# Kernel optimization log

Measured on AMD Instinct MI355X. Metric: run time of the kernel, lower is better.

Reference implementation:

```python
import jax, jax.numpy as jnp
import numpy as np
import math

B, T, C = 8, 2048, 1024
N_LAYER, LAYER_ID = 24, 12


def setup_inputs() -> dict:
    key = jax.random.key(0)
    ks = jax.random.split(key, 8)
    # deterministic parameter init, mirroring RWKV_TimeMix.__init__
    ratio_0_to_1 = LAYER_ID / (N_LAYER - 1)
    ratio_1_to_almost0 = 1.0 - LAYER_ID / N_LAYER
    h = np.arange(C, dtype=np.float64)
    time_decay = (-5 + 8 * (h / (C - 1)) ** (0.7 + 1.3 * ratio_0_to_1)).astype(np.float32)
    zigzag = (np.array([(i + 1) % 3 - 1 for i in range(C)], dtype=np.float64) * 0.5)
    time_first = (np.ones(C) * math.log(0.3) + zigzag).astype(np.float32)
    xpos = (np.arange(C, dtype=np.float64) / C)
    time_mix_k = (xpos ** ratio_1_to_almost0).astype(np.float32).reshape(1, 1, C)
    time_mix_v = (xpos ** ratio_1_to_almost0 + 0.3 * ratio_0_to_1).astype(np.float32).reshape(1, 1, C)
    time_mix_r = (xpos ** (0.5 * ratio_1_to_almost0)).astype(np.float32).reshape(1, 1, C)
    scale = 1.0 / math.sqrt(C)
    return {
        "x": jax.random.normal(ks[0], (B, T, C), jnp.float32),
        "time_decay": jnp.asarray(time_decay),
        "time_first": jnp.asarray(time_first),
        "time_mix_k": jnp.asarray(time_mix_k),
        "time_mix_v": jnp.asarray(time_mix_v),
        "time_mix_r": jnp.asarray(time_mix_r),
        "Wk": jax.random.normal(ks[1], (C, C), jnp.float32) * scale,
        "Wv": jax.random.normal(ks[2], (C, C), jnp.float32) * scale,
        "Wr": jax.random.normal(ks[3], (C, C), jnp.float32) * scale,
        "Wo": jax.random.normal(ks[4], (C, C), jnp.float32) * scale,
    }


def wkv_scan(w_decay, u, k, v):
    """Numerically-stable RWKV-4 WKV recurrence.
    w_decay, u: [C]; k, v: [B, T, C]. Returns [B, T, C].
    """
    w = -jnp.exp(w_decay)  # negative decay per channel
    kt = jnp.swapaxes(k, 0, 1)  # [T, B, C]
    vt = jnp.swapaxes(v, 0, 1)
    Bn, Cn = k.shape[0], k.shape[2]
    aa0 = jnp.zeros((Bn, Cn), k.dtype)
    bb0 = jnp.zeros((Bn, Cn), k.dtype)
    pp0 = jnp.full((Bn, Cn), -1e38, k.dtype)

    def step(carry, kv):
        aa, bb, pp = carry
        k_t, v_t = kv
        ww = u + k_t
        q = jnp.maximum(pp, ww)
        e1 = jnp.exp(pp - q)
        e2 = jnp.exp(ww - q)
        y = (e1 * aa + e2 * v_t) / (e1 * bb + e2)
        ww2 = pp + w
        q2 = jnp.maximum(ww2, k_t)
        e1 = jnp.exp(ww2 - q2)
        e2 = jnp.exp(k_t - q2)
        return (e1 * aa + e2 * v_t, e1 * bb + e2, q2), y

    _, ys = jax.lax.scan(step, (aa0, bb0, pp0), (kt, vt))
    return jnp.swapaxes(ys, 0, 1)  # [B, T, C]


def reference(x, time_decay, time_first, time_mix_k, time_mix_v, time_mix_r, Wk, Wv, Wr, Wo):
    # time shift: x_{t-1}, zero at t=0
    xx = jnp.pad(x, ((0, 0), (1, 0), (0, 0)))[:, :-1]
    xk = x * time_mix_k + xx * (1.0 - time_mix_k)
    xv = x * time_mix_v + xx * (1.0 - time_mix_v)
    xr = x * time_mix_r + xx * (1.0 - time_mix_r)
    k = jnp.einsum("btc,oc->bto", xk, Wk)
    v = jnp.einsum("btc,oc->bto", xv, Wv)
    r = jnp.einsum("btc,oc->bto", xr, Wr)
    wkv = wkv_scan(time_decay, time_first, k, v)
    rwkv = jax.nn.sigmoid(r) * wkv
    return jnp.einsum("btc,oc->bto", rwkv, Wo)
```

## Files before the change

kernel.cpp:

```cpp
#include <hip/hip_runtime.h>

#define BB 8
#define TT 2048
#define CC 1024
#define WKV_L 64
#define WKV_NCH (TT / WKV_L)

typedef __bf16 bf16x8_t __attribute__((ext_vector_type(8)));
typedef float f32x4_t __attribute__((ext_vector_type(4)));

__device__ __forceinline__ unsigned short f2bf(float f) {
  unsigned u = __float_as_uint(f);
  u += 0x7fffu + ((u >> 16) & 1u);
  return (unsigned short)(u >> 16);
}
__device__ __forceinline__ float bf2f(unsigned short s) {
  return __uint_as_float(((unsigned)s) << 16);
}

#define GLOAD16(gp, lp)                                                        \
  __builtin_amdgcn_global_load_lds(                                            \
      (const __attribute__((address_space(1))) void*)(gp),                     \
      (__attribute__((address_space(3))) void*)(lp), 16, 0, 0)

__global__ __launch_bounds__(256) void mix2_cast_kernel(
    const float* __restrict__ x, const float* __restrict__ tmk,
    const float* __restrict__ tmv,
    unsigned short* __restrict__ xk, unsigned short* __restrict__ xv) {
  const size_t total4 = (size_t)BB * TT * CC / 4;
  for (size_t i = (size_t)blockIdx.x * blockDim.x + threadIdx.x; i < total4;
       i += (size_t)gridDim.x * blockDim.x) {
    size_t e = i * 4;
    int c = (int)(e & (CC - 1));
    int t = (int)((e / CC) & (TT - 1));
    float4 xv4 = ((const float4*)x)[i];
    float4 xp = make_float4(0.f, 0.f, 0.f, 0.f);
    if (t > 0) xp = ((const float4*)x)[i - CC / 4];
    float4 mk = *(const float4*)(tmk + c);
    float4 mv = *(const float4*)(tmv + c);
    ushort4 ok, ov;
    ok.x = f2bf(xv4.x * mk.x + xp.x * (1.f - mk.x));
    ok.y = f2bf(xv4.y * mk.y + xp.y * (1.f - mk.y));
    ok.z = f2bf(xv4.z * mk.z + xp.z * (1.f - mk.z));
    ok.w = f2bf(xv4.w * mk.w + xp.w * (1.f - mk.w));
    ov.x = f2bf(xv4.x * mv.x + xp.x * (1.f - mv.x));
    ov.y = f2bf(xv4.y * mv.y + xp.y * (1.f - mv.y));
    ov.z = f2bf(xv4.z * mv.z + xp.z * (1.f - mv.z));
    ov.w = f2bf(xv4.w * mv.w + xp.w * (1.f - mv.w));
    *(ushort4*)(xk + e) = ok;
    *(ushort4*)(xv + e) = ov;
  }
}

__global__ __launch_bounds__(256) void mix_cast_kernel(const float* __restrict__ x,
                                const float* __restrict__ tmix,
                                unsigned short* __restrict__ out) {
  const size_t total4 = (size_t)BB * TT * CC / 4;
  for (size_t i = (size_t)blockIdx.x * blockDim.x + threadIdx.x; i < total4;
       i += (size_t)gridDim.x * blockDim.x) {
    size_t e = i * 4;
    int c = (int)(e & (CC - 1));
    int t = (int)((e / CC) & (TT - 1));
    float4 xv = ((const float4*)x)[i];
    float4 xp = make_float4(0.f, 0.f, 0.f, 0.f);
    if (t > 0) xp = ((const float4*)x)[i - CC / 4];
    float4 tm = *(const float4*)(tmix + c);
    ushort4 o;
    o.x = f2bf(xv.x * tm.x + xp.x * (1.f - tm.x));
    o.y = f2bf(xv.y * tm.y + xp.y * (1.f - tm.y));
    o.z = f2bf(xv.z * tm.z + xp.z * (1.f - tm.z));
    o.w = f2bf(xv.w * tm.w + xp.w * (1.f - tm.w));
    *(ushort4*)(out + e) = o;
  }
}

__global__ __launch_bounds__(256) void cast_w4_kernel(
    const float* __restrict__ w0, const float* __restrict__ w1,
    const float* __restrict__ w2, const float* __restrict__ w3,
    unsigned short* __restrict__ o0, unsigned short* __restrict__ o1,
    unsigned short* __restrict__ o2, unsigned short* __restrict__ o3) {
  const int n4 = CC * CC / 4;
  for (int i = blockIdx.x * blockDim.x + threadIdx.x; i < 4 * n4;
       i += gridDim.x * blockDim.x) {
    int sel = i / n4;
    int j = i - sel * n4;
    const float* w = sel == 0 ? w0 : sel == 1 ? w1 : sel == 2 ? w2 : w3;
    unsigned short* o = sel == 0 ? o0 : sel == 1 ? o1 : sel == 2 ? o2 : o3;
    float4 v = ((const float4*)w)[j];
    ushort4 u;
    u.x = f2bf(v.x); u.y = f2bf(v.y); u.z = f2bf(v.z); u.w = f2bf(v.w);
    ((ushort4*)o)[j] = u;
  }
}

#define NT8 (CC / 64)

template <typename EPI>
__device__ __forceinline__ void gemm8_body(unsigned short* lds8,
                                           const unsigned short* __restrict__ A,
                                           const unsigned short* __restrict__ Bm,
                                           int tm, int tn, EPI epi) {
  const int tid = threadIdx.x;
  const int lane = tid & 63;
  const int wid = tid >> 6;
  const int wr = wid >> 2;
  const int wc = wid & 3;
  const int fr = lane & 15;
  const int fk = lane >> 4;

  const int srow = tid >> 3;
  const int gcol = (((tid & 7) ^ (srow & 7)) << 3);
  const unsigned short* Ag = A + (size_t)(tm * 256 + srow) * CC + gcol;
  const unsigned short* Bg = Bm + (size_t)(tn * 256 + srow) * CC + gcol;
  const int ldst = tid << 3;

  const int rowA = wr * 16 + fr;
  const int rowB = wc * 16 + fr;
  const int sx0 = ((fk ^ (fr & 7)) << 3);
  const int sx1 = (((4 + fk) ^ (fr & 7)) << 3);

  bf16x8_t aF[4][2];
  bf16x8_t bF[2][2][2];
  f32x4_t acc[8][4] = {};

#define STG_A(T, H)                                                            \
  {                                                                            \
    const unsigned short* g_ = Ag + (size_t)((H) * 128) * CC + (T) * 64;       \
    unsigned short* l_ = &lds8[(((T) & 1) << 14) + (H) * 8192 + ldst];         \
    GLOAD16(g_, l_);                                                           \
    GLOAD16(g_ + (size_t)64 * CC, l_ + 4096);                                  \
  }
#define STG_B(T, H)                                                            \
  {                                                                            \
    const unsigned short* g_ = Bg + (size_t)((H) * 128) * CC + (T) * 64;       \
    unsigned short* l_ = &lds8[32768 + (((T) & 1) << 14) + (H) * 8192 + ldst]; \
    GLOAD16(g_, l_);                                                           \
    GLOAD16(g_ + (size_t)64 * CC, l_ + 4096);                                  \
  }
#define LOADA(MH)                                                              \
  _Pragma("unroll") for (int i_ = 0; i_ < 4; ++i_) {                           \
    aF[i_][0] = *(const bf16x8_t*)&lds8[ab + ((MH) * 4 + i_) * 2048 + sx0];    \
    aF[i_][1] = *(const bf16x8_t*)&lds8[ab + ((MH) * 4 + i_) * 2048 + sx1];    \
  }
#define LOADB(NH)                                                              \
  _Pragma("unroll") for (int j_ = 0; j_ < 2; ++j_) {                           \
    bF[NH][j_][0] = *(const bf16x8_t*)&lds8[bb + ((NH) * 2 + j_) * 4096 + sx0];\
    bF[NH][j_][1] = *(const bf16x8_t*)&lds8[bb + ((NH) * 2 + j_) * 4096 + sx1];\
  }
#define MFMAQ(MH, NH)                                                          \
  _Pragma("unroll") for (int i_ = 0; i_ < 4; ++i_)                             \
  _Pragma("unroll") for (int j_ = 0; j_ < 2; ++j_) {                           \
    acc[(MH) * 4 + i_][(NH) * 2 + j_] = __builtin_amdgcn_mfma_f32_16x16x32_bf16( \
        aF[i_][0], bF[NH][j_][0], acc[(MH) * 4 + i_][(NH) * 2 + j_], 0, 0, 0); \
    acc[(MH) * 4 + i_][(NH) * 2 + j_] = __builtin_amdgcn_mfma_f32_16x16x32_bf16( \
        aF[i_][1], bF[NH][j_][1], acc[(MH) * 4 + i_][(NH) * 2 + j_], 0, 0, 0); \
  }

  STG_A(0, 0) STG_B(0, 0) STG_A(0, 1) STG_B(0, 1)
  STG_A(1, 0) STG_B(1, 0) STG_A(1, 1)
  asm volatile("s_waitcnt vmcnt(10)" ::: "memory");
  __builtin_amdgcn_s_barrier();

#pragma unroll
  for (int t = 0; t < NT8; ++t) {
    const int ab = ((t & 1) << 14) + rowA * 64;
    const int bb = 32768 + ((t & 1) << 14) + rowB * 64;
    LOADA(0) LOADB(0)
    if (t + 1 < NT8) { STG_B(t + 1, 1) }
    asm volatile("s_waitcnt vmcnt(8)" ::: "memory");
    __builtin_amdgcn_s_barrier();
    __builtin_amdgcn_s_setprio(1);
    MFMAQ(0, 0)
    __builtin_amdgcn_s_setprio(0);
    __builtin_amdgcn_s_barrier();
    LOADB(1)
    if (t + 2 < NT8) { STG_A(t + 2, 0) }
    __builtin_amdgcn_s_barrier();
    __builtin_amdgcn_s_setprio(1);
    MFMAQ(0, 1)
    __builtin_amdgcn_s_setprio(0);
    __builtin_amdgcn_s_barrier();
    LOADA(1)
    if (t + 2 < NT8) { STG_B(t + 2, 0) }
    __builtin_amdgcn_s_barrier();
    __builtin_amdgcn_s_setprio(1);
    MFMAQ(1, 0)
    __builtin_amdgcn_s_setprio(0);
    __builtin_amdgcn_s_barrier();
    if (t + 2 < NT8) { STG_A(t + 2, 1) }
    asm volatile("s_waitcnt vmcnt(10)" ::: "memory");
    __builtin_amdgcn_s_barrier();
    __builtin_amdgcn_s_setprio(1);
    MFMAQ(1, 1)
    __builtin_amdgcn_s_setprio(0);
    __builtin_amdgcn_s_barrier();
  }

#pragma unroll
  for (int im = 0; im < 8; ++im)
#pragma unroll
    for (int jn = 0; jn < 4; ++jn)
#pragma unroll
      for (int rg = 0; rg < 4; ++rg)
        epi((size_t)(tm * 256 + wr * 16 + im * 32 + (fk << 2) + rg) * CC +
                (size_t)(tn * 256 + wc * 16 + jn * 64 + fr),
            acc[im][jn][rg]);
#undef STG_A
#undef STG_B
#undef LOADA
#undef LOADB
#undef MFMAQ
}

template <int OUT_BF16>
__global__ __launch_bounds__(512, 2) void gemm8_one(const unsigned short* __restrict__ A,
                         const unsigned short* __restrict__ Bm,
                         void* __restrict__ Cm) {
  __shared__ unsigned short lds8[65536];
  int orig = blockIdx.x;
  int wg = (orig & 7) * 32 + (orig >> 3);
  int tm = wg >> 2;
  int tn = wg & 3;
  if (OUT_BF16)
    gemm8_body(lds8, A, Bm, tm, tn,
               [&](size_t off, float val) { ((unsigned short*)Cm)[off] = f2bf(val); });
  else
    gemm8_body(lds8, A, Bm, tm, tn,
               [&](size_t off, float val) { ((float*)Cm)[off] = val; });
}

__global__ __launch_bounds__(256) void wkv_phase1(const float* __restrict__ k,
                           const unsigned short* __restrict__ v,
                           const float* __restrict__ wdec,
                           float* __restrict__ Sa, float* __restrict__ Sb,
                           float* __restrict__ Sp) {
  int idx = blockIdx.x * blockDim.x + threadIdx.x;
  int c = idx & (CC - 1);
  int bj = idx >> 10;
  int j = bj % WKV_NCH;
  int b = bj / WKV_NCH;
  float w = -__expf(wdec[c]);
  size_t base = (size_t)b * TT * CC + (size_t)j * WKV_L * CC + c;
  float aa = 0.f, bb = 0.f, pp = -1e38f;
  for (int t = 0; t < WKV_L; ++t) {
    size_t off = base + (size_t)t * CC;
    float kt = k[off];
    float vt = bf2f(v[off]);
    float ww2 = pp + w;
    float q2 = fmaxf(ww2, kt);
    float f1 = __expf(ww2 - q2);
    float f2 = __expf(kt - q2);
    aa = fmaf(f1, aa, f2 * vt);
    bb = fmaf(f1, bb, f2);
    pp = q2;
  }
  Sa[idx] = aa; Sb[idx] = bb; Sp[idx] = pp;
}

__global__ __launch_bounds__(256) void wkv_phase2(const float* __restrict__ wdec,
                           const float* __restrict__ Sa, const float* __restrict__ Sb,
                           const float* __restrict__ Sp,
                           float* __restrict__ Ia, float* __restrict__ Ib,
                           float* __restrict__ Ip) {
  int idx = blockIdx.x * blockDim.x + threadIdx.x;
  if (idx >= BB * CC) return;
  int c = idx & (CC - 1);
  int b = idx >> 10;
  float wL = -__expf(wdec[c]) * (float)WKV_L;
  float aa = 0.f, bb = 0.f, pp = -1e38f;
  for (int j = 0; j < WKV_NCH; ++j) {
    size_t s = (size_t)(b * WKV_NCH + j) * CC + c;
    Ia[s] = aa; Ib[s] = bb; Ip[s] = pp;
    float pd = pp + wL;
    float ps = Sp[s];
    float q = fmaxf(pd, ps);
    float e1 = __expf(pd - q);
    float e2 = __expf(ps - q);
    aa = fmaf(e1, aa, e2 * Sa[s]);
    bb = fmaf(e1, bb, e2 * Sb[s]);
    pp = q;
  }
}

__global__ __launch_bounds__(256) void wkv_phase3(const float* __restrict__ k,
                           const unsigned short* __restrict__ v,
                           const unsigned short* r,
                           const float* __restrict__ wdec,
                           const float* __restrict__ u,
                           const float* __restrict__ Ia, const float* __restrict__ Ib,
                           const float* __restrict__ Ip,
                           unsigned short* out) {
  int idx = blockIdx.x * blockDim.x + threadIdx.x;
  int c = idx & (CC - 1);
  int bj = idx >> 10;
  int j = bj % WKV_NCH;
  int b = bj / WKV_NCH;
  float w = -__expf(wdec[c]);
  float uu = u[c];
  float aa = Ia[idx], bb = Ib[idx], pp = Ip[idx];
  size_t base = (size_t)b * TT * CC + (size_t)j * WKV_L * CC + c;
  for (int t = 0; t < WKV_L; ++t) {
    size_t off = base + (size_t)t * CC;
    float kt = k[off];
    float vt = bf2f(v[off]);
    float ww = uu + kt;
    float q = fmaxf(pp, ww);
    float e1 = __expf(pp - q);
    float e2 = __expf(ww - q);
    float y = fmaf(e1, aa, e2 * vt) / fmaf(e1, bb, e2);
    float ww2 = pp + w;
    float q2 = fmaxf(ww2, kt);
    float f1 = __expf(ww2 - q2);
    float f2 = __expf(kt - q2);
    aa = fmaf(f1, aa, f2 * vt);
    bb = fmaf(f1, bb, f2);
    pp = q2;
    float rt = bf2f(r[off]);
    float sr = 1.f / (1.f + __expf(-rt));
    out[off] = f2bf(sr * y);
  }
}

extern "C" void kernel_launch(void* const* d_in, const int* in_sizes, int n_in,
                              void* d_out, int out_size, void* d_ws, size_t ws_size,
                              hipStream_t stream) {
  const float* x    = (const float*)d_in[0];
  const float* tdec = (const float*)d_in[1];
  const float* tfir = (const float*)d_in[2];
  const float* tmk  = (const float*)d_in[3];
  const float* tmv  = (const float*)d_in[4];
  const float* tmr  = (const float*)d_in[5];
  const float* Wk   = (const float*)d_in[6];
  const float* Wv   = (const float*)d_in[7];
  const float* Wr   = (const float*)d_in[8];
  const float* Wo   = (const float*)d_in[9];

  const size_t M = (size_t)BB * TT;
  const size_t mixbytes = M * CC * 2;
  const size_t wbytes = (size_t)CC * CC * 2;
  const size_t nstate = (size_t)BB * WKV_NCH * CC;

  char* ws = (char*)d_ws;
  unsigned short* xkb = (unsigned short*)ws;  ws += mixbytes;
  unsigned short* xvb = (unsigned short*)ws;  ws += mixbytes;
  unsigned short* rbuf = xvb;
  unsigned short* Wkb = (unsigned short*)ws; ws += wbytes;
  unsigned short* Wvb = (unsigned short*)ws; ws += wbytes;
  unsigned short* Wrb = (unsigned short*)ws; ws += wbytes;
  unsigned short* Wob = (unsigned short*)ws; ws += wbytes;
  float* kbuf = (float*)ws;                   ws += M * CC * 4;
  unsigned short* vbuf = (unsigned short*)ws; ws += mixbytes;
  float* Sa = (float*)ws; ws += nstate * 4;
  float* Sb = (float*)ws; ws += nstate * 4;
  float* Sp = (float*)ws; ws += nstate * 4;
  float* Ia = (float*)ws; ws += nstate * 4;
  float* Ib = (float*)ws; ws += nstate * 4;
  float* Ip = (float*)ws; ws += nstate * 4;

  dim3 blk(256);
  dim3 blk8(512);
  const int wkv_grid = (int)(nstate / 256);

  cast_w4_kernel<<<1024, blk, 0, stream>>>(Wk, Wv, Wr, Wo, Wkb, Wvb, Wrb, Wob);
  mix2_cast_kernel<<<2048, blk, 0, stream>>>(x, tmk, tmv, xkb, xvb);
  gemm8_one<0><<<256, blk8, 0, stream>>>(xkb, Wkb, kbuf);
  gemm8_one<1><<<256, blk8, 0, stream>>>(xvb, Wvb, vbuf);
  mix_cast_kernel<<<2048, blk, 0, stream>>>(x, tmr, xkb);
  gemm8_one<1><<<256, blk8, 0, stream>>>(xkb, Wrb, rbuf);

  wkv_phase1<<<wkv_grid, blk, 0, stream>>>(kbuf, vbuf, tdec, Sa, Sb, Sp);
  wkv_phase2<<<(BB * CC + 255) / 256, blk, 0, stream>>>(tdec, Sa, Sb, Sp, Ia, Ib, Ip);
  wkv_phase3<<<wkv_grid, blk, 0, stream>>>(kbuf, vbuf, rbuf, tdec, tfir,
                                           Ia, Ib, Ip, rbuf);

  gemm8_one<0><<<256, blk8, 0, stream>>>(rbuf, Wob, d_out);
}
```

Baseline: 273.9 us.

## Use lazy-rescale WKV recurrence, halve chunk length, fuse r mix into one kernel

Replaces the two-max, four-exp WKV step with a lazily rescaled form that needs one exp per step plus a rare rescale branch, and clamps the output exponent. The chunk length drops from 64 to 32, which doubles the number of parallel chunks in phases 1 and 3 and doubles the serial length of phase 2. The r time-mix is computed in the same pass as k and v, writing to a third buffer, so x is read one fewer time. The lazy rescale allows accumulators to grow up to about e^8 before renormalising, and the clamp at 60 alters numerics for extreme inputs.

Measured after the change: 258.7 us. 5.6% less time.

```diff
diff --git a/kernel.cpp b/kernel.cpp
--- a/kernel.cpp
+++ b/kernel.cpp
@@ -3,8 +3,9 @@
 #define BB 8
 #define TT 2048
 #define CC 1024
-#define WKV_L 64
+#define WKV_L 32
 #define WKV_NCH (TT / WKV_L)
+#define WKV_LOG_NCH 6
 
 typedef __bf16 bf16x8_t __attribute__((ext_vector_type(8)));
 typedef float f32x4_t __attribute__((ext_vector_type(4)));
@@ -23,10 +24,11 @@
       (const __attribute__((address_space(1))) void*)(gp),                     \
       (__attribute__((address_space(3))) void*)(lp), 16, 0, 0)
 
-__global__ __launch_bounds__(256) void mix2_cast_kernel(
+__global__ __launch_bounds__(256) void mix3_cast_kernel(
     const float* __restrict__ x, const float* __restrict__ tmk,
-    const float* __restrict__ tmv,
-    unsigned short* __restrict__ xk, unsigned short* __restrict__ xv) {
+    const float* __restrict__ tmv, const float* __restrict__ tmr,
+    unsigned short* __restrict__ xk, unsigned short* __restrict__ xv,
+    unsigned short* __restrict__ xr) {
   const size_t total4 = (size_t)BB * TT * CC / 4;
   for (size_t i = (size_t)blockIdx.x * blockDim.x + threadIdx.x; i < total4;
        i += (size_t)gridDim.x * blockDim.x) {
@@ -38,7 +40,8 @@
     if (t > 0) xp = ((const float4*)x)[i - CC / 4];
     float4 mk = *(const float4*)(tmk + c);
     float4 mv = *(const float4*)(tmv + c);
-    ushort4 ok, ov;
+    float4 mr = *(const float4*)(tmr + c);
+    ushort4 ok, ov, orr;
     ok.x = f2bf(xv4.x * mk.x + xp.x * (1.f - mk.x));
     ok.y = f2bf(xv4.y * mk.y + xp.y * (1.f - mk.y));
     ok.z = f2bf(xv4.z * mk.z + xp.z * (1.f - mk.z));
@@ -47,30 +50,13 @@
     ov.y = f2bf(xv4.y * mv.y + xp.y * (1.f - mv.y));
     ov.z = f2bf(xv4.z * mv.z + xp.z * (1.f - mv.z));
     ov.w = f2bf(xv4.w * mv.w + xp.w * (1.f - mv.w));
+    orr.x = f2bf(xv4.x * mr.x + xp.x * (1.f - mr.x));
+    orr.y = f2bf(xv4.y * mr.y + xp.y * (1.f - mr.y));
+    orr.z = f2bf(xv4.z * mr.z + xp.z * (1.f - mr.z));
+    orr.w = f2bf(xv4.w * mr.w + xp.w * (1.f - mr.w));
     *(ushort4*)(xk + e) = ok;
     *(ushort4*)(xv + e) = ov;
-  }
-}
-
-__global__ __launch_bounds__(256) void mix_cast_kernel(const float* __restrict__ x,
-                                const float* __restrict__ tmix,
-                                unsigned short* __restrict__ out) {
-  const size_t total4 = (size_t)BB * TT * CC / 4;
-  for (size_t i = (size_t)blockIdx.x * blockDim.x + threadIdx.x; i < total4;
-       i += (size_t)gridDim.x * blockDim.x) {
-    size_t e = i * 4;
-    int c = (int)(e & (CC - 1));
-    int t = (int)((e / CC) & (TT - 1));
-    float4 xv = ((const float4*)x)[i];
-    float4 xp = make_float4(0.f, 0.f, 0.f, 0.f);
-    if (t > 0) xp = ((const float4*)x)[i - CC / 4];
-    float4 tm = *(const float4*)(tmix + c);
-    ushort4 o;
-    o.x = f2bf(xv.x * tm.x + xp.x * (1.f - tm.x));
-    o.y = f2bf(xv.y * tm.y + xp.y * (1.f - tm.y));
-    o.z = f2bf(xv.z * tm.z + xp.z * (1.f - tm.z));
-    o.w = f2bf(xv.w * tm.w + xp.w * (1.f - tm.w));
-    *(ushort4*)(out + e) = o;
+    *(ushort4*)(xr + e) = orr;
   }
 }
 
@@ -237,22 +223,24 @@
   int idx = blockIdx.x * blockDim.x + threadIdx.x;
   int c = idx & (CC - 1);
   int bj = idx >> 10;
-  int j = bj % WKV_NCH;
-  int b = bj / WKV_NCH;
+  int j = bj & (WKV_NCH - 1);
+  int b = bj >> WKV_LOG_NCH;
   float w = -__expf(wdec[c]);
-  size_t base = (size_t)b * TT * CC + (size_t)j * WKV_L * CC + c;
+  size_t base = ((size_t)b * TT + (size_t)j * WKV_L) * CC + c;
   float aa = 0.f, bb = 0.f, pp = -1e38f;
   for (int t = 0; t < WKV_L; ++t) {
     size_t off = base + (size_t)t * CC;
     float kt = k[off];
     float vt = bf2f(v[off]);
-    float ww2 = pp + w;
-    float q2 = fmaxf(ww2, kt);
-    float f1 = __expf(ww2 - q2);
-    float f2 = __expf(kt - q2);
-    aa = fmaf(f1, aa, f2 * vt);
-    bb = fmaf(f1, bb, f2);
-    pp = q2;
+    pp += w;
+    float d = kt - pp;
+    if (d > 8.f) {
+      float s = __expf(-d);
+      aa *= s; bb *= s; pp = kt; d = 0.f;
+    }
+    float E = __expf(d);
+    aa = fmaf(E, vt, aa);
+    bb += E;
   }
   Sa[idx] = aa; Sb[idx] = bb; Sp[idx] = pp;
 }
@@ -293,31 +281,31 @@
   int idx = blockIdx.x * blockDim.x + threadIdx.x;
   int c = idx & (CC - 1);
   int bj = idx >> 10;
-  int j = bj % WKV_NCH;
-  int b = bj / WKV_NCH;
+  int j = bj & (WKV_NCH - 1);
+  int b = bj >> WKV_LOG_NCH;
   float w = -__expf(wdec[c]);
   float uu = u[c];
   float aa = Ia[idx], bb = Ib[idx], pp = Ip[idx];
-  size_t base = (size_t)b * TT * CC + (size_t)j * WKV_L * CC + c;
+  size_t base = ((size_t)b * TT + (size_t)j * WKV_L) * CC + c;
   for (int t = 0; t < WKV_L; ++t) {
     size_t off = base + (size_t)t * CC;
     float kt = k[off];
     float vt = bf2f(v[off]);
-    float ww = uu + kt;
-    float q = fmaxf(pp, ww);
-    float e1 = __expf(pp - q);
-    float e2 = __expf(ww - q);
-    float y = fmaf(e1, aa, e2 * vt) / fmaf(e1, bb, e2);
-    float ww2 = pp + w;
-    float q2 = fmaxf(ww2, kt);
-    float f1 = __expf(ww2 - q2);
-    float f2 = __expf(kt - q2);
-    aa = fmaf(f1, aa, f2 * vt);
-    bb = fmaf(f1, bb, f2);
-    pp = q2;
+    float dy = fminf(uu + kt - pp, 60.f);
+    float Eu = __expf(dy);
+    float y = fmaf(Eu, vt, aa) / (bb + Eu);
     float rt = bf2f(r[off]);
     float sr = 1.f / (1.f + __expf(-rt));
     out[off] = f2bf(sr * y);
+    pp += w;
+    float d = kt - pp;
+    if (d > 8.f) {
+      float s = __expf(-d);
+      aa *= s; bb *= s; pp = kt; d = 0.f;
+    }
+    float E = __expf(d);
+    aa = fmaf(E, vt, aa);
+    bb += E;
   }
 }
 
@@ -343,7 +331,8 @@
   char* ws = (char*)d_ws;
   unsigned short* xkb = (unsigned short*)ws;  ws += mixbytes;
   unsigned short* xvb = (unsigned short*)ws;  ws += mixbytes;
-  unsigned short* rbuf = xvb;
+  unsigned short* xrb = (unsigned short*)ws;  ws += mixbytes;
+  unsigned short* rbuf = xkb;
   unsigned short* Wkb = (unsigned short*)ws; ws += wbytes;
   unsigned short* Wvb = (unsigned short*)ws; ws += wbytes;
   unsigned short* Wrb = (unsigned short*)ws; ws += wbytes;
@@ -362,11 +351,10 @@
   const int wkv_grid = (int)(nstate / 256);
 
   cast_w4_kernel<<<1024, blk, 0, stream>>>(Wk, Wv, Wr, Wo, Wkb, Wvb, Wrb, Wob);
-  mix2_cast_kernel<<<2048, blk, 0, stream>>>(x, tmk, tmv, xkb, xvb);
+  mix3_cast_kernel<<<2048, blk, 0, stream>>>(x, tmk, tmv, tmr, xkb, xvb, xrb);
   gemm8_one<0><<<256, blk8, 0, stream>>>(xkb, Wkb, kbuf);
   gemm8_one<1><<<256, blk8, 0, stream>>>(xvb, Wvb, vbuf);
-  mix_cast_kernel<<<2048, blk, 0, stream>>>(x, tmr, xkb);
-  gemm8_one<1><<<256, blk8, 0, stream>>>(xkb, Wrb, rbuf);
+  gemm8_one<1><<<256, blk8, 0, stream>>>(xrb, Wrb, rbuf);
 
   wkv_phase1<<<wkv_grid, blk, 0, stream>>>(kbuf, vbuf, tdec, Sa, Sb, Sp);
   wkv_phase2<<<(BB * CC + 255) / 256, blk, 0, stream>>>(tdec, Sa, Sb, Sp, Ia, Ib, Ip);
```
